# Kernel optimization log

Measured on AMD Instinct MI355X. Metric: run time of the kernel, lower is better.

The kernel has to match this reference:

```python
import jax, jax.numpy as jnp
import numpy as np

M, C, K, D = 2048, 16, 8, 256  # queries, classes, clusters/class, feature_dim
H1, H2 = D, D // 2             # MLP hidden sizes


def setup_inputs() -> dict:
    key = jax.random.key(0)
    ks = jax.random.split(key, 8)
    s1 = 1.0 / np.sqrt(2 * D)
    s2 = 1.0 / np.sqrt(H1)
    s3 = 1.0 / np.sqrt(H2)
    return {
        "query_features": jax.random.normal(ks[0], (M, D), jnp.float32),
        "prototypes": jax.random.normal(ks[1], (C, K, D), jnp.float32),
        "W1": jax.random.normal(ks[2], (2 * D, H1), jnp.float32) * s1,
        "b1": jnp.zeros((H1,), jnp.float32),
        "W2": jax.random.normal(ks[3], (H1, H2), jnp.float32) * s2,
        "b2": jnp.zeros((H2,), jnp.float32),
        "W3": jax.random.normal(ks[4], (H2, 1), jnp.float32) * s3,
        "b3": jnp.zeros((1,), jnp.float32),
    }


def reference(query_features, prototypes, W1, b1, W2, b2, W3, b3):
    # Attention MLP on concat([query, prototype]) for every (query, class, cluster)
    # pair. Split W1 into the query half and prototype half so we never
    # materialize the [M,C,K,2D] concat; broadcast-add instead.
    d = query_features.shape[-1]
    Wq, Wp = W1[:d], W1[d:]
    qh = query_features @ Wq                      # [M, H1]
    ph = jnp.einsum('ckd,dh->ckh', prototypes, Wp)  # [C, K, H1]
    h = jax.nn.relu(qh[:, None, None, :] + ph[None] + b1)   # [M, C, K, H1]
    h = jax.nn.relu(h @ W2 + b2)                              # [M, C, K, H2]
    scores = (h @ W3)[..., 0] + b3[0]                         # [M, C, K]
    attn = jax.nn.softmax(scores, axis=-1)                    # softmax over clusters
    weighted = jnp.einsum('mck,ckd->mcd', attn, prototypes)   # [M, C, D]
    diff = query_features[:, None, :] - weighted              # [M, C, D]
    distances = jnp.sqrt(jnp.sum(diff * diff, axis=-1))       # [M, C]
    return -distances
```

## Files before the change

### kernel.cpp

```cpp
#include <hip/hip_runtime.h>
#include <hip/hip_fp16.h>
#include <cstdint>

typedef __attribute__((ext_vector_type(8))) _Float16 f16x8;
typedef __attribute__((ext_vector_type(4))) float f32x4;
typedef __attribute__((ext_vector_type(16))) float f32x16;

__device__ __forceinline__ f16x8 cvt8(float4 x, float4 y) {
    f16x8 r;
    r[0] = (_Float16)x.x; r[1] = (_Float16)x.y; r[2] = (_Float16)x.z; r[3] = (_Float16)x.w;
    r[4] = (_Float16)y.x; r[5] = (_Float16)y.y; r[6] = (_Float16)y.z; r[7] = (_Float16)y.w;
    return r;
}

__device__ __forceinline__ f16x8 relu8(f16x8 v) {
    f16x8 z = {};
    return __builtin_elementwise_max(v, z);
}

__global__ __launch_bounds__(256, 2)
void prep1(const float* __restrict__ query,
           const float* __restrict__ prot,
           const float* __restrict__ W1,
           const float* __restrict__ b1,
           const float* __restrict__ W2,
           const float* __restrict__ b2,
           _Float16* __restrict__ qh16,
           float* __restrict__ sqp,
           _Float16* __restrict__ phpk,
           f16x8* __restrict__ w2p,
           float* __restrict__ Gm,
           float* __restrict__ q2) {
    __shared__ _Float16 Bls[64][280];
    int b = blockIdx.x, t = threadIdx.x;

    if (b < 200) {
        int mode, row0, col0;
        if (b < 128)      { mode = 0; row0 = (b >> 2) * 64;         col0 = (b & 3) * 64; }
        else if (b < 192) { mode = 1; row0 = ((b - 128) >> 1) * 64; col0 = ((b - 128) & 1) * 64; }
        else              { mode = 2; row0 = ((b - 192) >> 2) * 64; col0 = ((b - 192) & 3) * 64; }
        const float* Asrc = (mode == 2) ? prot : query;

        if (mode != 1) {
            int woff = (mode == 2) ? 256 : 0;
            int rr = t >> 4, c4 = (t & 15) * 4;
            for (int rt = 0; rt < 4; ++rt) {
                #pragma unroll
                for (int it = 0; it < 4; ++it) {
                    int k = rt * 64 + it * 16 + rr;
                    float4 v = *(const float4*)(W1 + (woff + k) * 256 + col0 + c4);
                    Bls[c4 + 0][k] = (_Float16)v.x;
                    Bls[c4 + 1][k] = (_Float16)v.y;
                    Bls[c4 + 2][k] = (_Float16)v.z;
                    Bls[c4 + 3][k] = (_Float16)v.w;
                }
            }
            __syncthreads();
        }

        int w = t >> 6, l = t & 63, l15 = l & 15, l4 = l >> 4;
        f32x4 acc[4];
        #pragma unroll
        for (int nt = 0; nt < 4; ++nt) acc[nt] = (f32x4){0.f, 0.f, 0.f, 0.f};

        for (int ks = 0; ks < 8; ++ks) {
            int row = row0 + w * 16 + l15;
            const float* ap = Asrc + row * 256 + ks * 32 + l4 * 8;
            f16x8 af = cvt8(*(const float4*)ap, *(const float4*)(ap + 4));
            f16x8 bf[4];
            #pragma unroll
            for (int nt = 0; nt < 4; ++nt) {
                if (mode == 1) {
                    int col = col0 + nt * 16 + l15;
                    const float* bp = prot + col * 256 + ks * 32 + l4 * 8;
                    bf[nt] = cvt8(*(const float4*)bp, *(const float4*)(bp + 4));
                } else {
                    bf[nt] = *(const f16x8*)(&Bls[nt * 16 + l15][ks * 32 + l4 * 8]);
                }
            }
            #pragma unroll
            for (int nt = 0; nt < 4; ++nt)
                acc[nt] = __builtin_amdgcn_mfma_f32_16x16x32_f16(af, bf[nt], acc[nt], 0, 0, 0);
        }
        #pragma unroll
        for (int nt = 0; nt < 4; ++nt)
            #pragma unroll
            for (int j = 0; j < 4; ++j) {
                int row = row0 + w * 16 + l4 * 4 + j;
                int col = col0 + nt * 16 + l15;
                float v = acc[nt][j];
                if (mode == 0) {
                    _Float16 v16 = (_Float16)v;
                    __builtin_nontemporal_store(v16, &qh16[row * 256 + col]);
                } else if (mode == 1) {
                    __builtin_nontemporal_store(v, &sqp[row * 128 + col]);
                } else {
                    _Float16 v16 = (_Float16)(v + b1[col]);
                    __builtin_nontemporal_store(v16,
                        &phpk[(((col >> 4) * 2 + ((col >> 3) & 1)) * 128 + row) * 8 + (col & 7)]);
                }
            }
    } else if (b < 217) {
        int chunk = (b - 200) * 256 + t;
        int ks = chunk >> 8, h = (chunk >> 7) & 1, c = chunk & 127;
        f16x8 o = {};
        if (ks < 16) {
            #pragma unroll
            for (int j = 0; j < 8; ++j)
                o[j] = (_Float16)W2[(ks * 16 + h * 8 + j) * 128 + c];
        } else if (h == 0) {
            o[0] = (_Float16)b2[c];
        }
        __builtin_nontemporal_store(o, &w2p[chunk]);
    } else if (b < 249) {
        int pid = (b - 217) * 32 + (t >> 3), l8 = t & 7;
        int c = pid >> 6, k = (pid >> 3) & 7, kp = pid & 7;
        const float4* pa = (const float4*)(prot + (c * 8 + k) * 256 + l8 * 32);
        const float4* pb = (const float4*)(prot + (c * 8 + kp) * 256 + l8 * 32);
        float s = 0.f;
        #pragma unroll
        for (int i = 0; i < 8; ++i) {
            float4 x = pa[i], y = pb[i];
            s += x.x * y.x + x.y * y.y + x.z * y.z + x.w * y.w;
        }
        s += __shfl_xor(s, 1); s += __shfl_xor(s, 2); s += __shfl_xor(s, 4);
        if (l8 == 0) __builtin_nontemporal_store(s, &Gm[pid]);
    } else {
        int m = (b - 249) * 32 + (t >> 3), l8 = t & 7;
        const float4* qp = (const float4*)(query + m * 256 + l8 * 32);
        float s = 0.f;
        #pragma unroll
        for (int i = 0; i < 8; ++i) {
            float4 x = qp[i];
            s += x.x * x.x + x.y * x.y + x.z * x.z + x.w * x.w;
        }
        s += __shfl_xor(s, 1); s += __shfl_xor(s, 2); s += __shfl_xor(s, 4);
        if (l8 == 0) __builtin_nontemporal_store(s, &q2[m]);
    }
}

__global__ __launch_bounds__(256, 1)
void fused7(const _Float16* __restrict__ qh16,
            const uint4* __restrict__ phpk,
            const uint4* __restrict__ w2p,
            const float* __restrict__ sqp,
            const float* __restrict__ q2,
            const float* __restrict__ Gm,
            const float* __restrict__ W3,
            const float* __restrict__ b2,
            float* __restrict__ out) {
    __shared__ _Float16 qlds[8 * 256];
    __shared__ uint4 phl[1024];
    __shared__ float w3l[128];
    __shared__ float b2l[128];
    __shared__ float sql[8 * 32];
    __shared__ float gml[256];
    __shared__ float q2l[8];
    __shared__ float spart[2][2][4][32];

    int t = threadIdx.x;
    int cs = t >> 6, l = t & 63;
    int lk = l & 31, h = l >> 5;
    int cks = blockIdx.x & 3;
    int mg = blockIdx.x >> 2;
    int m0 = mg * 8;

    const _Float16* w2h = (const _Float16*)w2p;

    ((uint4*)qlds)[t] = ((const uint4*)(qh16 + m0 * 256))[t];
    #pragma unroll
    for (int i = 0; i < 4; ++i) {
        int j = t + i * 256;
        phl[j] = phpk[(j >> 5) * 128 + cks * 32 + (j & 31)];
    }
    if (t < 128) { w3l[t] = W3[t]; b2l[t] = b2[t]; }
    {
        int rloc = t >> 5, c = t & 31;
        sql[t] = __builtin_nontemporal_load(&sqp[(m0 + rloc) * 128 + cks * 32 + c]);
        gml[t] = Gm[cks * 256 + t];
        if (t < 8) q2l[t] = q2[m0 + t];
    }

    f16x8 wA[16];
    #pragma unroll
    for (int ks = 0; ks < 16; ++ks)
        wA[ks] = *(const f16x8*)(w2h + ((ks * 2 + h) * 128 + cs * 32 + lk) * 8);

    __syncthreads();

    const f16x8* phlh = (const f16x8*)phl;

    for (int pass = 0; pass < 4; ++pass) {
        const _Float16* qr0 = qlds + (pass * 2) * 256 + h * 8;
        const _Float16* qr1 = qr0 + 256;

        f32x16 acc0 = {}, acc1 = {};

        f16x8 qv0[2], qv1[2];
        #pragma unroll
        for (int p = 0; p < 2; ++p) {
            qv0[p] = *(const f16x8*)(qr0 + p * 16);
            qv1[p] = *(const f16x8*)(qr1 + p * 16);
        }

        #pragma unroll
        for (int ks = 0; ks < 16; ++ks) {
            f16x8 phf = phlh[(ks * 2 + h) * 32 + lk];
            f16x8 a0 = relu8(qv0[ks & 1] + phf);
            f16x8 a1 = relu8(qv1[ks & 1] + phf);
            if (ks < 14) {
                qv0[ks & 1] = *(const f16x8*)(qr0 + (ks + 2) * 16);
                qv1[ks & 1] = *(const f16x8*)(qr1 + (ks + 2) * 16);
            }
            acc0 = __builtin_amdgcn_mfma_f32_32x32x16_f16(wA[ks], a0, acc0, 0, 0, 0);
            acc1 = __builtin_amdgcn_mfma_f32_32x32x16_f16(wA[ks], a1, acc1, 0, 0, 0);
        }

        int buf = pass & 1;
        auto score1 = [&](const f32x16& A) -> float {
            float s0 = 0.f, s1 = 0.f, s2 = 0.f, s3 = 0.f;
            #pragma unroll
            for (int r = 0; r < 16; r += 4) {
                int c0i = cs * 32 + ((r + 0) & 3) + 8 * ((r + 0) >> 2) + 4 * h;
                int c1i = cs * 32 + ((r + 1) & 3) + 8 * ((r + 1) >> 2) + 4 * h;
                int c2i = cs * 32 + ((r + 2) & 3) + 8 * ((r + 2) >> 2) + 4 * h;
                int c3i = cs * 32 + ((r + 3) & 3) + 8 * ((r + 3) >> 2) + 4 * h;
                s0 = fmaf(fmaxf(A[r + 0] + b2l[c0i], 0.f), w3l[c0i], s0);
                s1 = fmaf(fmaxf(A[r + 1] + b2l[c1i], 0.f), w3l[c1i], s1);
                s2 = fmaf(fmaxf(A[r + 2] + b2l[c2i], 0.f), w3l[c2i], s2);
                s3 = fmaf(fmaxf(A[r + 3] + b2l[c3i], 0.f), w3l[c3i], s3);
            }
            float s = (s0 + s1) + (s2 + s3);
            s += __shfl_xor(s, 32);
            return s;
        };
        float sc0 = score1(acc0);
        float sc1 = score1(acc1);
        if (l < 32) {
            spart[buf][0][cs][lk] = sc0;
            spart[buf][1][cs][lk] = sc1;
        }
        __syncthreads();

        if (t < 64) {
            int msel = t >> 5, cl = t & 31, kk = t & 7;
            int rloc = pass * 2 + msel;
            int m = m0 + rloc;
            int cgl = cl >> 3;
            float s = spart[buf][msel][0][cl] + spart[buf][msel][1][cl]
                    + spart[buf][msel][2][cl] + spart[buf][msel][3][cl];
            float mx = s;
            mx = fmaxf(mx, __shfl_xor(mx, 1));
            mx = fmaxf(mx, __shfl_xor(mx, 2));
            mx = fmaxf(mx, __shfl_xor(mx, 4));
            float e = __expf(s - mx);
            float den = e;
            den += __shfl_xor(den, 1); den += __shfl_xor(den, 2); den += __shfl_xor(den, 4);
            float a = e / den;
            float p2 = a * sql[rloc * 32 + cl];
            float p3 = 0.f;
            #pragma unroll
            for (int kq = 0; kq < 8; ++kq) {
                float ak = __shfl(a, (l & 56) | kq);
                p3 = fmaf(ak, gml[cgl * 64 + kq * 8 + kk], p3);
            }
            p3 *= a;
            float pr = p3 - 2.f * p2;
            pr += __shfl_xor(pr, 1); pr += __shfl_xor(pr, 2); pr += __shfl_xor(pr, 4);
            if (kk == 0)
                out[m * 16 + cks * 4 + cgl] = -sqrtf(fmaxf(q2l[rloc] + pr, 0.f));
        }
    }
}

extern "C" void kernel_launch(void* const* d_in, const int* in_sizes, int n_in,
                              void* d_out, int out_size, void* d_ws, size_t ws_size,
                              hipStream_t stream) {
    const float* query = (const float*)d_in[0];
    const float* prot  = (const float*)d_in[1];
    const float* W1    = (const float*)d_in[2];
    const float* b1    = (const float*)d_in[3];
    const float* W2    = (const float*)d_in[4];
    const float* b2    = (const float*)d_in[5];
    const float* W3    = (const float*)d_in[6];

    char* ws = (char*)d_ws;
    _Float16* qh16 = (_Float16*)(ws);
    f16x8*    w2p  = (f16x8*)(ws + 1048576);
    _Float16* phpk = (_Float16*)(ws + 1118208);
    float*    sqp  = (float*)(ws + 1183744);
    float*    q2   = (float*)(ws + 2232320);
    float*    Gm   = (float*)(ws + 2240512);
    float* out = (float*)d_out;

    prep1<<<313, 256, 0, stream>>>(query, prot, W1, b1, W2, b2,
                                   qh16, sqp, phpk, w2p, Gm, q2);
    fused7<<<1024, 256, 0, stream>>>(qh16, (const uint4*)phpk, (const uint4*)w2p,
                                     sqp, q2, Gm, W3, b2, out);
}
```

Baseline: 40.50 us.

## Give each wave a full query row and stage W2 in LDS instead

Reorganizes the fused MLP kernel so each wave computes all four 32-column H2 slices for its own query row. The per-wave prototype activations stay in registers and W2 is streamed from a 64KB LDS copy. This removes the cross-wave partial-score exchange and the block-wide syncs inside the pass loop, and lets every wave do its own softmax and distance epilogue. Each block now covers 16 queries, so half as many blocks launch, with larger LDS use per block and more LDS reads of W2 per MFMA.

```diff
diff --git a/kernel.cpp b/kernel.cpp
--- a/kernel.cpp
+++ b/kernel.cpp
@@ -140,7 +140,7 @@
 }
 
 __global__ __launch_bounds__(256, 1)
-void fused7(const _Float16* __restrict__ qh16,
+void fused8(const _Float16* __restrict__ qh16,
             const uint4* __restrict__ phpk,
             const uint4* __restrict__ w2p,
             const float* __restrict__ sqp,
@@ -149,127 +149,100 @@
             const float* __restrict__ W3,
             const float* __restrict__ b2,
             float* __restrict__ out) {
-    __shared__ _Float16 qlds[8 * 256];
-    __shared__ uint4 phl[1024];
+    __shared__ uint4 w2l[4096];
+    __shared__ _Float16 qlds[16 * 256];
+    __shared__ float sql[16 * 32];
+    __shared__ float gml[256];
     __shared__ float w3l[128];
     __shared__ float b2l[128];
-    __shared__ float sql[8 * 32];
-    __shared__ float gml[256];
-    __shared__ float q2l[8];
-    __shared__ float spart[2][2][4][32];
+    __shared__ float q2l[16];
 
     int t = threadIdx.x;
-    int cs = t >> 6, l = t & 63;
+    int wid = t >> 6, l = t & 63;
     int lk = l & 31, h = l >> 5;
     int cks = blockIdx.x & 3;
     int mg = blockIdx.x >> 2;
-    int m0 = mg * 8;
-
-    const _Float16* w2h = (const _Float16*)w2p;
-
-    ((uint4*)qlds)[t] = ((const uint4*)(qh16 + m0 * 256))[t];
+    int m0 = mg * 16;
+
     #pragma unroll
-    for (int i = 0; i < 4; ++i) {
-        int j = t + i * 256;
-        phl[j] = phpk[(j >> 5) * 128 + cks * 32 + (j & 31)];
+    for (int i = 0; i < 16; ++i) w2l[t + i * 256] = w2p[t + i * 256];
+    ((uint4*)qlds)[t]       = ((const uint4*)(qh16 + m0 * 256))[t];
+    ((uint4*)qlds)[t + 256] = ((const uint4*)(qh16 + m0 * 256))[t + 256];
+    {
+        int r0 = t >> 5, c0 = t & 31;
+        sql[t]       = sqp[(m0 + r0) * 128 + cks * 32 + c0];
+        sql[t + 256] = sqp[(m0 + 8 + r0) * 128 + cks * 32 + c0];
+        gml[t & 255] = Gm[cks * 256 + (t & 255)];
     }
     if (t < 128) { w3l[t] = W3[t]; b2l[t] = b2[t]; }
-    {
-        int rloc = t >> 5, c = t & 31;
-        sql[t] = __builtin_nontemporal_load(&sqp[(m0 + rloc) * 128 + cks * 32 + c]);
-        gml[t] = Gm[cks * 256 + t];
-        if (t < 8) q2l[t] = q2[m0 + t];
-    }
-
-    f16x8 wA[16];
+    if (t < 16) q2l[t] = q2[m0 + t];
+
+    f16x8 ph[16];
     #pragma unroll
     for (int ks = 0; ks < 16; ++ks)
-        wA[ks] = *(const f16x8*)(w2h + ((ks * 2 + h) * 128 + cs * 32 + lk) * 8);
+        ph[ks] = ((const f16x8*)phpk)[(ks * 2 + h) * 128 + cks * 32 + lk];
 
     __syncthreads();
 
-    const f16x8* phlh = (const f16x8*)phl;
+    const _Float16* w2lh = (const _Float16*)w2l;
 
     for (int pass = 0; pass < 4; ++pass) {
-        const _Float16* qr0 = qlds + (pass * 2) * 256 + h * 8;
-        const _Float16* qr1 = qr0 + 256;
-
-        f32x16 acc0 = {}, acc1 = {};
-
-        f16x8 qv0[2], qv1[2];
-        #pragma unroll
-        for (int p = 0; p < 2; ++p) {
-            qv0[p] = *(const f16x8*)(qr0 + p * 16);
-            qv1[p] = *(const f16x8*)(qr1 + p * 16);
-        }
+        int mloc = wid * 4 + pass;
+        int m = m0 + mloc;
+        const _Float16* qr = qlds + mloc * 256 + h * 8;
+
+        f32x16 acc[4];
+        #pragma unroll
+        for (int s = 0; s < 4; ++s) acc[s] = (f32x16){};
+
+        f16x8 qv[2];
+        qv[0] = *(const f16x8*)(qr);
+        qv[1] = *(const f16x8*)(qr + 16);
 
         #pragma unroll
         for (int ks = 0; ks < 16; ++ks) {
-            f16x8 phf = phlh[(ks * 2 + h) * 32 + lk];
-            f16x8 a0 = relu8(qv0[ks & 1] + phf);
-            f16x8 a1 = relu8(qv1[ks & 1] + phf);
-            if (ks < 14) {
-                qv0[ks & 1] = *(const f16x8*)(qr0 + (ks + 2) * 16);
-                qv1[ks & 1] = *(const f16x8*)(qr1 + (ks + 2) * 16);
-            }
-            acc0 = __builtin_amdgcn_mfma_f32_32x32x16_f16(wA[ks], a0, acc0, 0, 0, 0);
-            acc1 = __builtin_amdgcn_mfma_f32_32x32x16_f16(wA[ks], a1, acc1, 0, 0, 0);
-        }
-
-        int buf = pass & 1;
-        auto score1 = [&](const f32x16& A) -> float {
-            float s0 = 0.f, s1 = 0.f, s2 = 0.f, s3 = 0.f;
-            #pragma unroll
-            for (int r = 0; r < 16; r += 4) {
-                int c0i = cs * 32 + ((r + 0) & 3) + 8 * ((r + 0) >> 2) + 4 * h;
-                int c1i = cs * 32 + ((r + 1) & 3) + 8 * ((r + 1) >> 2) + 4 * h;
-                int c2i = cs * 32 + ((r + 2) & 3) + 8 * ((r + 2) >> 2) + 4 * h;
-                int c3i = cs * 32 + ((r + 3) & 3) + 8 * ((r + 3) >> 2) + 4 * h;
-                s0 = fmaf(fmaxf(A[r + 0] + b2l[c0i], 0.f), w3l[c0i], s0);
-                s1 = fmaf(fmaxf(A[r + 1] + b2l[c1i], 0.f), w3l[c1i], s1);
-                s2 = fmaf(fmaxf(A[r + 2] + b2l[c2i], 0.f), w3l[c2i], s2);
-                s3 = fmaf(fmaxf(A[r + 3] + b2l[c3i], 0.f), w3l[c3i], s3);
-            }
-            float s = (s0 + s1) + (s2 + s3);
-            s += __shfl_xor(s, 32);
-            return s;
-        };
-        float sc0 = score1(acc0);
-        float sc1 = score1(acc1);
-        if (l < 32) {
-            spart[buf][0][cs][lk] = sc0;
-            spart[buf][1][cs][lk] = sc1;
-        }
-        __syncthreads();
-
-        if (t < 64) {
-            int msel = t >> 5, cl = t & 31, kk = t & 7;
-            int rloc = pass * 2 + msel;
-            int m = m0 + rloc;
-            int cgl = cl >> 3;
-            float s = spart[buf][msel][0][cl] + spart[buf][msel][1][cl]
-                    + spart[buf][msel][2][cl] + spart[buf][msel][3][cl];
-            float mx = s;
-            mx = fmaxf(mx, __shfl_xor(mx, 1));
-            mx = fmaxf(mx, __shfl_xor(mx, 2));
-            mx = fmaxf(mx, __shfl_xor(mx, 4));
-            float e = __expf(s - mx);
-            float den = e;
-            den += __shfl_xor(den, 1); den += __shfl_xor(den, 2); den += __shfl_xor(den, 4);
-            float a = e / den;
-            float p2 = a * sql[rloc * 32 + cl];
-            float p3 = 0.f;
-            #pragma unroll
-            for (int kq = 0; kq < 8; ++kq) {
-                float ak = __shfl(a, (l & 56) | kq);
-                p3 = fmaf(ak, gml[cgl * 64 + kq * 8 + kk], p3);
-            }
-            p3 *= a;
-            float pr = p3 - 2.f * p2;
-            pr += __shfl_xor(pr, 1); pr += __shfl_xor(pr, 2); pr += __shfl_xor(pr, 4);
-            if (kk == 0)
-                out[m * 16 + cks * 4 + cgl] = -sqrtf(fmaxf(q2l[rloc] + pr, 0.f));
-        }
+            f16x8 act = relu8(qv[ks & 1] + ph[ks]);
+            if (ks < 14)
+                qv[ks & 1] = *(const f16x8*)(qr + (ks + 2) * 16);
+            #pragma unroll
+            for (int s = 0; s < 4; ++s) {
+                f16x8 bfr = *(const f16x8*)(w2lh + ((ks * 2 + h) * 128 + s * 32 + lk) * 8);
+                acc[s] = __builtin_amdgcn_mfma_f32_32x32x16_f16(bfr, act, acc[s], 0, 0, 0);
+            }
+        }
+
+        float sc = 0.f;
+        #pragma unroll
+        for (int s = 0; s < 4; ++s)
+            #pragma unroll
+            for (int r = 0; r < 16; ++r) {
+                int ci = s * 32 + (r & 3) + 8 * (r >> 2) + 4 * h;
+                sc = fmaf(fmaxf(acc[s][r] + b2l[ci], 0.f), w3l[ci], sc);
+            }
+        sc += __shfl_xor(sc, 32);
+
+        float mx = sc;
+        mx = fmaxf(mx, __shfl_xor(mx, 1));
+        mx = fmaxf(mx, __shfl_xor(mx, 2));
+        mx = fmaxf(mx, __shfl_xor(mx, 4));
+        float e = __expf(sc - mx);
+        float den = e;
+        den += __shfl_xor(den, 1); den += __shfl_xor(den, 2); den += __shfl_xor(den, 4);
+        float a = e / den;
+
+        int kk = l & 7, cgl = lk >> 3;
+        float p2 = a * sql[mloc * 32 + lk];
+        float p3 = 0.f;
+        #pragma unroll
+        for (int kq = 0; kq < 8; ++kq) {
+            float ak = __shfl(a, (l & 56) | kq);
+            p3 = fmaf(ak, gml[cgl * 64 + kq * 8 + kk], p3);
+        }
+        p3 *= a;
+        float pr = p3 - 2.f * p2;
+        pr += __shfl_xor(pr, 1); pr += __shfl_xor(pr, 2); pr += __shfl_xor(pr, 4);
+        if (l < 32 && kk == 0)
+            out[m * 16 + cks * 4 + cgl] = -sqrtf(fmaxf(q2l[mloc] + pr, 0.f));
     }
 }
 
@@ -295,6 +268,6 @@
 
     prep1<<<313, 256, 0, stream>>>(query, prot, W1, b1, W2, b2,
                                    qh16, sqp, phpk, w2p, Gm, q2);
-    fused7<<<1024, 256, 0, stream>>>(qh16, (const uint4*)phpk, (const uint4*)w2p,
-                                     sqp, q2, Gm, W3, b2, out);
-}
+    fused8<<<512, 256, 0, stream>>>(qh16, (const uint4*)phpk, (const uint4*)w2p,
+                                    sqp, q2, Gm, W3, b2, out);
+}
```

After: 53.60 us. +32.4%, slower.
